# Optimization experiments

Hardware: AMD Instinct MI355X
Metric: run time of the kernel (lower is better)

Reference implementation:

```python
import jax, jax.numpy as jnp
import numpy as np

N = 2048      # agent_num
H = 2048      # hid_size
OBS = 1024    # obs_size
A = 64        # action_dim
ITERS = 3     # comm_iters
B = 1         # batch (structurally 1: original does gate.view(1,n,n))
STD = 0.02


def setup_inputs() -> dict:
    key = jax.random.key(0)
    ks = jax.random.split(key, 10)
    f = lambda k, shp: (jax.random.normal(k, shp, jnp.float32) * STD)
    return {
        "obs": jax.random.normal(ks[0], (B, N, OBS), jnp.float32),
        "alive_mask": jnp.ones((N,), jnp.float32),
        "enc_w": f(ks[1], (H, OBS)),
        "enc_b": jnp.zeros((H,), jnp.float32),
        "g_w": f(ks[2], (N, H)),
        "g_b": jnp.zeros((N,), jnp.float32),
        "w_ih": f(ks[3], (4 * H, H)),
        "w_hh": f(ks[4], (4 * H, H)),
        "b_ih": f(ks[5], (4 * H,)),
        "b_hh": f(ks[6], (4 * H,)),
        "act_w": f(ks[7], (A, H)),
        "act_b": jnp.zeros((A,), jnp.float32),
        "val_w": f(ks[8], (1, H)),
        "val_b": jnp.zeros((1,), jnp.float32),
    }


def reference(obs, alive_mask, enc_w, enc_b, g_w, g_b, w_ih, w_hh,
              b_ih, b_hh, act_w, act_b, val_w, val_b):
    b, n, _ = obs.shape
    hid = enc_w.shape[0]
    # state encoder: tanh(Linear(obs))
    e = jnp.tanh(jnp.einsum('bno,ho->bnh', obs, enc_w) + enc_b)  # (B,n,H)
    h = jnp.zeros((b, n, hid), obs.dtype)
    cell = jnp.zeros((b, n, hid), obs.dtype)
    comm_mask = 1.0 - jnp.eye(n, dtype=obs.dtype)                # (n,n), no self-comm
    n_alive = jnp.sum(alive_mask)
    alive_pair = alive_mask[:, None] * alive_mask[None, :]       # alive[j]*alive[i]
    static_w = comm_mask * alive_pair / (n_alive - 1.0)          # (n,n)

    for it in range(ITERS):
        # hard gate: ceil(sigmoid(g(h)))  -> (B, n_sender, n_receiver)
        gate = jnp.ceil(jax.nn.sigmoid(jnp.einsum('bjh,kh->bjk', h, g_w) + g_b))
        G = gate * static_w                                      # (B,n,n)
        # masked gated broadcast-sum over sender agents j (fused, no (B,n,n,H))
        if it == 0:
            c = jnp.zeros_like(h)
        else:
            c = jnp.einsum('bji,bjh->bih', G, h)
        inp = e + c                                              # (B,n,H)
        # torch.nn.LSTMCell, gate order (i, f, g, o)
        z = (jnp.einsum('bnh,gh->bng', inp, w_ih)
             + jnp.einsum('bnh,gh->bng', h, w_hh) + b_ih + b_hh)
        zi, zf, zg, zo = jnp.split(z, 4, axis=-1)
        cell = jax.nn.sigmoid(zf) * cell + jax.nn.sigmoid(zi) * jnp.tanh(zg)
        h = jax.nn.sigmoid(zo) * jnp.tanh(cell)

    log_p = jax.nn.log_softmax(jnp.einsum('bnh,ah->bna', h, act_w) + act_b, axis=-1)
    value = jnp.einsum('bnh,vh->bnv', h, val_w) + val_b
    return log_p, value
```

## Files before the change

kernel.cpp:

```cpp
#include <hip/hip_runtime.h>
#include <cmath>

#define N_AG 2048
#define HID  2048
#define OBSD 1024
#define ACT  64
#define GATES (4*HID)

typedef short s16x8 __attribute__((ext_vector_type(8)));
typedef short s16x4 __attribute__((ext_vector_type(4)));
typedef float f32x4 __attribute__((ext_vector_type(4)));

__device__ __forceinline__ unsigned short f2bf(float f) {
  union { float f; unsigned u; } v; v.f = f;
  return (unsigned short)((v.u + 0x7FFFu + ((v.u >> 16) & 1u)) >> 16);
}
__device__ __forceinline__ float bf2f(unsigned short u) {
  union { float f; unsigned u; } v; v.u = ((unsigned)u) << 16;
  return v.f;
}
__device__ __forceinline__ float fsigm(float x) {
  return __builtin_amdgcn_rcpf(1.0f + __expf(-x));
}
__device__ __forceinline__ float ftanh(float x) {
  return 2.0f * __builtin_amdgcn_rcpf(1.0f + __expf(-2.0f * x)) - 1.0f;
}

__device__ __forceinline__ void gload16(const unsigned short* g, unsigned short* l) {
  __builtin_amdgcn_global_load_lds(
      (const __attribute__((address_space(1))) void*)g,
      (__attribute__((address_space(3))) void*)l, 16, 0, 0);
}


template <int MODE, int ACCS>
__global__ __launch_bounds__(512, 2) void gemm256(
    const unsigned short* __restrict__ A, const unsigned short* __restrict__ B,
    int K, int lda, int ldb,
    unsigned short* __restrict__ E1b, const float* __restrict__ q,
    const float* __restrict__ bc, float* __restrict__ cell,
    unsigned short* __restrict__ hN,
    const float* __restrict__ alive, float* __restrict__ S)
{
  __shared__ __align__(16) unsigned short As[32768];
  __shared__ __align__(16) unsigned short Bs[32768];

  const int tid  = threadIdx.x;
  const int lane = tid & 63;
  const int wave = tid >> 6;
  const int wm   = wave >> 2, wn = wave & 3;
  const int quad = lane >> 4, l16 = lane & 15, r7 = lane & 7;
  const long tileM = (long)blockIdx.y * 256;
  const long tileN = (long)blockIdx.x * 256;

  const unsigned scol  = (((lane & 7) ^ (lane >> 3)) * 8u);
  const unsigned aoffL = (unsigned)(tileM + wave * 8 + (lane >> 3)) * (unsigned)lda + scol;
  const unsigned boffL = (unsigned)(tileN + (wave >> 2) * 64 + (wave & 3) * 8 + (lane >> 3))
                           * (unsigned)ldb + scol;

#define ST_A(d, h, t) { \
    gload16(A + aoffL + (unsigned)((h) * 64) * (unsigned)lda + (unsigned)(t) * 64u, \
            &As[(d) * 16384 + (h) * 8192 + wave * 512]); \
    gload16(A + aoffL + (unsigned)(128 + (h) * 64) * (unsigned)lda + (unsigned)(t) * 64u, \
            &As[(d) * 16384 + (h) * 8192 + wave * 512 + 4096]); }
#define ST_B(d, h, t) { \
    gload16(B + boffL + (unsigned)((h) * 32) * (unsigned)ldb + (unsigned)(t) * 64u, \
            &Bs[(d) * 16384 + (h) * 8192 + wave * 512]); \
    gload16(B + boffL + (unsigned)(128 + (h) * 32) * (unsigned)ldb + (unsigned)(t) * 64u, \
            &Bs[(d) * 16384 + (h) * 8192 + wave * 512 + 4096]); }

  const int ax = wm * 4096 + l16 * 64;
  const int bx = wn * 2048 + l16 * 64;
  const int c0 = (quad ^ r7) * 8;
  const int c1 = ((4 + quad) ^ r7) * 8;

  s16x8 af0[4][2], af1[4][2], bA[2][2], bB[2][2];
  f32x4 acc[8][4] = {};

#define LD_A(d, Mh, dst) { const unsigned short* p_ = &As[(d) * 16384 + (Mh) * 8192 + ax]; \
    _Pragma("unroll") for (int ml = 0; ml < 4; ++ml) { \
      dst[ml][0] = *(const s16x8*)(p_ + ml * 1024 + c0); \
      dst[ml][1] = *(const s16x8*)(p_ + ml * 1024 + c1); } }
#define LD_B(d, Nh, dst) { const unsigned short* p_ = &Bs[(d) * 16384 + (Nh) * 8192 + bx]; \
    _Pragma("unroll") for (int nl = 0; nl < 2; ++nl) { \
      dst[nl][0] = *(const s16x8*)(p_ + nl * 1024 + c0); \
      dst[nl][1] = *(const s16x8*)(p_ + nl * 1024 + c1); } }
#define QMM(Mh, Nh, afv, bb) \
    _Pragma("unroll") for (int ks = 0; ks < 2; ++ks) \
    _Pragma("unroll") for (int ml = 0; ml < 4; ++ml) \
    _Pragma("unroll") for (int nl = 0; nl < 2; ++nl) \
      acc[(Mh) * 4 + ml][(Nh) * 2 + nl] = __builtin_amdgcn_mfma_f32_16x16x32_bf16( \
          afv[ml][ks], bb[nl][ks], acc[(Mh) * 4 + ml][(Nh) * 2 + nl], 0, 0, 0);
#define BAR  __builtin_amdgcn_s_barrier()
#define SCHB __builtin_amdgcn_sched_barrier(0)

  const int NT = K >> 6;

  ST_B(0, 0, 0); ST_A(0, 0, 0); ST_B(0, 1, 0); ST_A(0, 1, 0);
  asm volatile("s_waitcnt vmcnt(0)" ::: "memory");
  BAR;
  LD_A(0, 0, af0); LD_B(0, 0, bA);

  for (int t = 0; t < NT; ++t) {
    const int cur = t & 1, nxt = cur ^ 1;
    const bool s1 = (t + 1 < NT);
    LD_B(cur, 1, bB);
    if (s1) { ST_B(nxt, 0, t + 1); ST_A(nxt, 0, t + 1); }
    SCHB;
    __builtin_amdgcn_s_setprio(1); QMM(0, 0, af0, bA); __builtin_amdgcn_s_setprio(0);
    if (s1) { asm volatile("s_waitcnt vmcnt(4)" ::: "memory"); }
    else    { asm volatile("s_waitcnt vmcnt(0)" ::: "memory"); }
    BAR;
    LD_A(cur, 1, af1);
    if (s1) ST_B(nxt, 1, t + 1);
    SCHB;
    __builtin_amdgcn_s_setprio(1); QMM(0, 1, af0, bB); __builtin_amdgcn_s_setprio(0);
    if (s1) { asm volatile("s_waitcnt vmcnt(2)" ::: "memory"); }
    BAR;
    if (s1) ST_A(nxt, 1, t + 1);
    SCHB;
    __builtin_amdgcn_s_setprio(1); QMM(1, 0, af1, bA); __builtin_amdgcn_s_setprio(0);
    if (s1) LD_B(nxt, 0, bA);
    BAR;
    if (s1) LD_A(nxt, 0, af0);
    SCHB;
    __builtin_amdgcn_s_setprio(1); QMM(1, 1, af1, bB); __builtin_amdgcn_s_setprio(0);
    if (s1) { asm volatile("s_waitcnt vmcnt(2)" ::: "memory"); }
    BAR;
  }

  const int cb0 = (int)tileN + wn * 64;
  const int hid = ((cb0 >> 6) << 4) | l16;
  const int bid = (int)blockIdx.y * (int)gridDim.x + (int)blockIdx.x;
  float bcv[4], qv[4];
#pragma unroll
  for (int g = 0; g < 4; ++g) {
    bcv[g] = bc[cb0 + g * 16 + l16];
    qv[g]  = (MODE == 11) ? q[cb0 + g * 16 + l16] : 0.f;
  }
  float sacc = 0.f;
#pragma unroll
  for (int mf = 0; mf < 8; ++mf) {
    long ag0 = tileM + wm * 128 + mf * 16 + quad * 4;
#pragma unroll
    for (int r = 0; r < 4; ++r) {
      long ag = ag0 + r;
      const size_t pk = ((size_t)bid * 32 + (mf * 4 + r)) * 512 + tid;
      float zi = acc[mf][0][r], zf = acc[mf][1][r];
      float zg = acc[mf][2][r], zo = acc[mf][3][r];
      if (MODE == 10) {
        s16x4 ev;
        ev[0] = (short)f2bf(zi); ev[1] = (short)f2bf(zf);
        ev[2] = (short)f2bf(zg); ev[3] = (short)f2bf(zo);
        *(s16x4*)&E1b[pk * 4] = ev;
        zi += bcv[0]; zf += bcv[1]; zg += bcv[2]; zo += bcv[3];
      } else {
        s16x4 ev = *(const s16x4*)&E1b[pk * 4];
        zi += bf2f((unsigned short)ev[0]) + qv[0] + bcv[0];
        zf += bf2f((unsigned short)ev[1]) + qv[1] + bcv[1];
        zg += bf2f((unsigned short)ev[2]) + qv[2] + bcv[2];
        zo += bf2f((unsigned short)ev[3]) + qv[3] + bcv[3];
      }
      float cold = (MODE == 10) ? 0.f : cell[pk];
      float cnew = fsigm(zf) * cold + fsigm(zi) * ftanh(zg);
      float hv   = fsigm(zo) * ftanh(cnew);
      cell[pk] = cnew;
      hN[(size_t)ag * HID + hid] = f2bf(hv);
      if (ACCS) sacc += alive[ag] * hv;
    }
  }
  if (ACCS) {
    sacc += __shfl_xor(sacc, 16);
    sacc += __shfl_xor(sacc, 32);
    if (quad == 0) atomicAdd(&S[hid], sacc);
  }
#undef ST_A
#undef ST_B
#undef LD_A
#undef LD_B
#undef QMM
#undef BAR
#undef SCHB
}

template <int MODE>
__global__ __launch_bounds__(256, 4) void gemm_bt(
    const unsigned short* __restrict__ A, const unsigned short* __restrict__ B,
    int K, int lda, int ldb,
    unsigned short* __restrict__ Cb, float* __restrict__ Cf, int ldc,
    const float* __restrict__ bias)
{
  __shared__ __align__(16) unsigned short As0[2 * 128 * 32];
  __shared__ __align__(16) unsigned short Bs0[2 * 128 * 32];
  const int tid  = threadIdx.x;
  const int lane = tid & 63;
  const int wave = tid >> 6;
  const int wm = wave >> 1, wn = wave & 1;
  const int quad = lane >> 4, l16 = lane & 15;
  const long tileM = (long)blockIdx.y * 128;
  const long tileN = (long)blockIdx.x * 128;
  const long koff  = (long)blockIdx.z * K;

  const int srow = lane >> 2;
  const int skc  = (lane & 3) * 8;
  const unsigned short* gA = &A[(tileM + wave * 32 + srow) * lda + koff + skc];
  const unsigned short* gB = &B[(tileN + wave * 32 + srow) * ldb + koff + skc];
  const int ldsOff = wave * 32 * 32;

  f32x4 acc[4][4] = {};
  const int nIt = K >> 5;

  gload16(gA, &As0[ldsOff]);
  gload16(gA + 16 * lda, &As0[ldsOff + 16 * 32]);
  gload16(gB, &Bs0[ldsOff]);
  gload16(gB + 16 * ldb, &Bs0[ldsOff + 16 * 32]);

  for (int i = 0; i < nIt; ++i) {
    __syncthreads();
    const int cb = (i & 1) * 4096;
    if (i + 1 < nIt) {
      const int nb = ((i + 1) & 1) * 4096;
      const long ko = (long)(i + 1) * 32;
      gload16(gA + ko, &As0[nb + ldsOff]);
      gload16(gA + ko + 16 * lda, &As0[nb + ldsOff + 16 * 32]);
      gload16(gB + ko, &Bs0[nb + ldsOff]);
      gload16(gB + ko + 16 * ldb, &Bs0[nb + ldsOff + 16 * 32]);
    }
    s16x8 af[4], bfr[4];
#pragma unroll
    for (int ii = 0; ii < 4; ++ii)
      af[ii] = *(const s16x8*)&As0[cb + (wm * 64 + ii * 16 + l16) * 32 + quad * 8];
#pragma unroll
    for (int j = 0; j < 4; ++j)
      bfr[j] = *(const s16x8*)&Bs0[cb + (wn * 64 + j * 16 + l16) * 32 + quad * 8];
#pragma unroll
    for (int ii = 0; ii < 4; ++ii)
#pragma unroll
      for (int j = 0; j < 4; ++j)
        acc[ii][j] = __builtin_amdgcn_mfma_f32_16x16x32_bf16(af[ii], bfr[j], acc[ii][j], 0, 0, 0);
  }

#pragma unroll
  for (int i = 0; i < 4; ++i) {
    long r0 = tileM + wm * 64 + i * 16 + quad * 4;
#pragma unroll
    for (int j = 0; j < 4; ++j) {
      long col = tileN + wn * 64 + j * 16 + l16;
      float bv = (MODE == 1) ? bias[col] : 0.f;
#pragma unroll
      for (int r = 0; r < 4; ++r) {
        float v = acc[i][j][r];
        if (MODE == 1) { v = ftanh(v + bv); Cb[(r0 + r) * ldc + col] = f2bf(v); }
        if (MODE == 2) atomicAdd(&Cf[(r0 + r) * ldc + col], v);
      }
    }
  }
}

__global__ void cvt4_dual(const float* __restrict__ inA, unsigned short* __restrict__ outA,
                          const float* __restrict__ inB, unsigned short* __restrict__ outB) {
  int i = blockIdx.x * 256 + threadIdx.x;
  f32x4 a = ((const f32x4*)inA)[i];
  f32x4 b = ((const f32x4*)inB)[i];
  s16x4 oa, ob;
#pragma unroll
  for (int c = 0; c < 4; ++c) { oa[c] = (short)f2bf(a[c]); ob[c] = (short)f2bf(b[c]); }
  ((s16x4*)outA)[i] = oa;
  ((s16x4*)outB)[i] = ob;
}

__global__ void buildw(const float* __restrict__ w_ih, const float* __restrict__ w_hh,
                       const float* __restrict__ nA,
                       unsigned short* __restrict__ Wihb, unsigned short* __restrict__ W2b) {
  int i = blockIdx.x * 256 + threadIdx.x;
  float s = 1.0f / (nA[0] - 1.0f);
  int c  = i >> 9;
  int kk = (i & 511) * 4;
  int g   = (c >> 4) & 3;
  int hid = ((c >> 6) << 4) | (c & 15);
  size_t src = ((size_t)g * HID + hid) * HID + kk;
  size_t dst = (size_t)c * HID + kk;
  f32x4 a = *(const f32x4*)&w_ih[src];
  f32x4 b = *(const f32x4*)&w_hh[src];
  s16x4 oa, ob;
#pragma unroll
  for (int e = 0; e < 4; ++e) {
    oa[e] = (short)f2bf(a[e]);
    ob[e] = (short)f2bf(b[e] - s * a[e]);
  }
  *(s16x4*)&Wihb[dst] = oa;
  *(s16x4*)&W2b[dst] = ob;
}

__global__ void build_whd(const float* __restrict__ act_w, const float* __restrict__ val_w,
                          unsigned short* __restrict__ whd) {
  int i = blockIdx.x * 256 + threadIdx.x;
  int r = i >> 9;
  int k = (i & 511) * 4;
  f32x4 v = {0.f, 0.f, 0.f, 0.f};
  if (r < 64)       v = *(const f32x4*)&act_w[(size_t)r * HID + k];
  else if (r == 64) v = *(const f32x4*)&val_w[k];
  s16x4 o;
  o[0] = (short)f2bf(v[0]); o[1] = (short)f2bf(v[1]);
  o[2] = (short)f2bf(v[2]); o[3] = (short)f2bf(v[3]);
  *(s16x4*)&whd[(size_t)r * HID + k] = o;
}

__global__ void biasmix(const float* __restrict__ b_ih, const float* __restrict__ b_hh,
                        float* __restrict__ bc) {
  int i = blockIdx.x * 256 + threadIdx.x;
  if (i < GATES) {
    int g   = (i >> 4) & 3;
    int hid = ((i >> 6) << 4) | (i & 15);
    int src = g * HID + hid;
    bc[i] = b_ih[src] + b_hh[src];
  }
}

__global__ void nalive_k(const float* __restrict__ alive, float* __restrict__ nA) {
  __shared__ float red[256];
  float s = 0.f;
  for (int i = threadIdx.x; i < N_AG; i += 256) s += alive[i];
  red[threadIdx.x] = s;
  __syncthreads();
  for (int st = 128; st > 0; st >>= 1) {
    if (threadIdx.x < st) red[threadIdx.x] += red[threadIdx.x + st];
    __syncthreads();
  }
  if (threadIdx.x == 0) nA[0] = red[0];
}

__global__ __launch_bounds__(256) void gemv_q(const unsigned short* __restrict__ Wihb,
                                              const float* __restrict__ S,
                                              const float* __restrict__ nA,
                                              float* __restrict__ q) {
  __shared__ float Sl[HID];
  int tid = threadIdx.x, lane = tid & 63, wave = tid >> 6;
  for (int k = tid; k < HID; k += 256) Sl[k] = S[k];
  __syncthreads();
  int g = blockIdx.x * 4 + wave;
  const unsigned short* wr = Wihb + (size_t)g * HID;
  float acc = 0.f;
#pragma unroll
  for (int c = 0; c < 4; ++c) {
    int k = c * 512 + lane * 8;
    s16x8 w = *(const s16x8*)&wr[k];
#pragma unroll
    for (int e = 0; e < 8; ++e) acc += bf2f((unsigned short)w[e]) * Sl[k + e];
  }
  for (int off = 32; off; off >>= 1) acc += __shfl_xor(acc, off);
  if (lane == 0) q[g] = acc / (nA[0] - 1.0f);
}

__global__ __launch_bounds__(256) void head_ep(const float* __restrict__ zh,
                                               const float* __restrict__ act_b,
                                               const float* __restrict__ val_b,
                                               float* __restrict__ out) {
  int wave = threadIdx.x >> 6, lane = threadIdx.x & 63;
  int row = blockIdx.x * 4 + wave;
  const float* zr = zh + (size_t)row * 128;
  float a = zr[lane] + act_b[lane];
  float m = a;
  for (int off = 32; off; off >>= 1) m = fmaxf(m, __shfl_xor(m, off));
  float ex = expf(a - m), s = ex;
  for (int off = 32; off; off >>= 1) s += __shfl_xor(s, off);
  out[(size_t)row * ACT + lane] = a - m - logf(s);
  if (lane == 0) out[(size_t)N_AG * ACT + row] = zr[64] + val_b[0];
}

extern "C" void kernel_launch(void* const* d_in, const int* in_sizes, int n_in,
                              void* d_out, int out_size, void* d_ws, size_t ws_size,
                              hipStream_t stream) {
  const float* obs   = (const float*)d_in[0];
  const float* alive = (const float*)d_in[1];
  const float* enc_w = (const float*)d_in[2];
  const float* enc_b = (const float*)d_in[3];
  const float* w_ih  = (const float*)d_in[6];
  const float* w_hh  = (const float*)d_in[7];
  const float* b_ih  = (const float*)d_in[8];
  const float* b_hh  = (const float*)d_in[9];
  const float* act_w = (const float*)d_in[10];
  const float* act_b = (const float*)d_in[11];
  const float* val_w = (const float*)d_in[12];
  const float* val_b = (const float*)d_in[13];
  float* out = (float*)d_out;

  char* p = (char*)d_ws;
  unsigned short* Wihb = (unsigned short*)p; p += (size_t)GATES * HID * 2;
  unsigned short* W2b  = (unsigned short*)p; p += (size_t)GATES * HID * 2;
  unsigned short* E1b  = (unsigned short*)p; p += (size_t)N_AG * GATES * 2;
  unsigned short* obsb = (unsigned short*)p; p += (size_t)N_AG * OBSD * 2;
  unsigned short* encb = (unsigned short*)p; p += (size_t)HID * OBSD * 2;
  unsigned short* eb   = (unsigned short*)p; p += (size_t)N_AG * HID * 2;
  unsigned short* h0   = (unsigned short*)p; p += (size_t)N_AG * HID * 2;
  unsigned short* h1   = (unsigned short*)p; p += (size_t)N_AG * HID * 2;
  unsigned short* Whd  = (unsigned short*)p; p += (size_t)128 * HID * 2;
  float* cell = (float*)p; p += (size_t)N_AG * HID * 4;
  float* zh   = (float*)p; p += (size_t)N_AG * 128 * 4;
  float* bc   = (float*)p; p += GATES * 4;
  float* q    = (float*)p; p += GATES * 4;
  float* S12  = (float*)p; p += 2 * HID * 4;
  float* nA   = (float*)p; p += 256;
  float* S1 = S12, *S2 = S12 + HID;

  cvt4_dual<<<(N_AG * OBSD / 4) / 256, 256, 0, stream>>>(obs, obsb, enc_w, encb);
  nalive_k<<<1, 256, 0, stream>>>(alive, nA);
  buildw<<<((size_t)GATES * HID / 4) / 256, 256, 0, stream>>>(w_ih, w_hh, nA, Wihb, W2b);
  build_whd<<<(128 * HID / 4) / 256, 256, 0, stream>>>(act_w, val_w, Whd);
  biasmix<<<GATES / 256, 256, 0, stream>>>(b_ih, b_hh, bc);
  hipMemsetAsync(S12, 0, 2 * HID * 4, stream);
  hipMemsetAsync(zh, 0, (size_t)N_AG * 128 * 4, stream);

  gemm_bt<1><<<dim3(HID / 128, N_AG / 128), 256, 0, stream>>>(
      obsb, encb, OBSD, OBSD, OBSD, eb, nullptr, HID, enc_b);

  gemm256<10, 1><<<dim3(GATES / 256, N_AG / 256), 512, 0, stream>>>(
      eb, Wihb, HID, HID, HID, E1b, nullptr, bc, cell, h0, alive, S1);

  gemv_q<<<GATES / 4, 256, 0, stream>>>(Wihb, S1, nA, q);
  gemm256<11, 1><<<dim3(GATES / 256, N_AG / 256), 512, 0, stream>>>(
      h0, W2b, HID, HID, HID, E1b, q, bc, cell, h1, alive, S2);

  gemv_q<<<GATES / 4, 256, 0, stream>>>(Wihb, S2, nA, q);
  gemm256<11, 0><<<dim3(GATES / 256, N_AG / 256), 512, 0, stream>>>(
      h1, W2b, HID, HID, HID, E1b, q, bc, cell, h0, alive, nullptr);

  gemm_bt<2><<<dim3(1, N_AG / 128, 8), 256, 0, stream>>>(
      h0, Whd, HID / 8, HID, HID, nullptr, zh, 128, nullptr);
  head_ep<<<N_AG / 4, 256, 0, stream>>>(zh, act_b, val_b, out);
}
```

Measured before the change: 477.6 us.

## Fuse prep kernels, swizzle block order, stage h stores through LDS

Merges the conversion, weight-build, bias-mix and memset launches into one prep kernel to cut launch overhead. Remaps block indices in gemm256 and the encoder GEMM so consecutive blocks share the same B (weight) tile, aiming for better L2 reuse. The LSTM epilogue now writes h into LDS and then emits coalesced 16-byte row stores instead of scattered 2-byte stores. The LDS staging adds a barrier and reuses the A buffer after the main loop.

```diff
diff --git a/kernel.cpp b/kernel.cpp
--- a/kernel.cpp
+++ b/kernel.cpp
@@ -50,8 +50,9 @@
   const int wave = tid >> 6;
   const int wm   = wave >> 2, wn = wave & 3;
   const int quad = lane >> 4, l16 = lane & 15, r7 = lane & 7;
-  const long tileM = (long)blockIdx.y * 256;
-  const long tileN = (long)blockIdx.x * 256;
+  const int lin  = (int)blockIdx.x + (int)blockIdx.y * (int)gridDim.x;
+  const long tileM = (long)(lin & 7) * 256;
+  const long tileN = (long)(lin >> 3) * 256;
 
   const unsigned scol  = (((lane & 7) ^ (lane >> 3)) * 8u);
   const unsigned aoffL = (unsigned)(tileM + wave * 8 + (lane >> 3)) * (unsigned)lda + scol;
@@ -130,14 +131,15 @@
   }
 
   const int cb0 = (int)tileN + wn * 64;
-  const int hid = ((cb0 >> 6) << 4) | l16;
-  const int bid = (int)blockIdx.y * (int)gridDim.x + (int)blockIdx.x;
+  const int hid0 = (int)(tileN >> 2);
+  const int bid = lin;
   float bcv[4], qv[4];
 #pragma unroll
   for (int g = 0; g < 4; ++g) {
     bcv[g] = bc[cb0 + g * 16 + l16];
     qv[g]  = (MODE == 11) ? q[cb0 + g * 16 + l16] : 0.f;
   }
+  unsigned short* hlds = As;
   float sacc = 0.f;
 #pragma unroll
   for (int mf = 0; mf < 8; ++mf) {
@@ -165,14 +167,22 @@
       float cnew = fsigm(zf) * cold + fsigm(zi) * ftanh(zg);
       float hv   = fsigm(zo) * ftanh(cnew);
       cell[pk] = cnew;
-      hN[(size_t)ag * HID + hid] = f2bf(hv);
+      hlds[(wm * 128 + mf * 16 + quad * 4 + r) * 64 + (wn * 16 + l16)] = f2bf(hv);
       if (ACCS) sacc += alive[ag] * hv;
     }
   }
   if (ACCS) {
     sacc += __shfl_xor(sacc, 16);
     sacc += __shfl_xor(sacc, 32);
-    if (quad == 0) atomicAdd(&S[hid], sacc);
+    if (quad == 0) atomicAdd(&S[hid0 + wn * 16 + l16], sacc);
+  }
+  __syncthreads();
+#pragma unroll
+  for (int k2 = 0; k2 < 4; ++k2) {
+    int ci = tid + 512 * k2;
+    int row = ci >> 3, c8 = ci & 7;
+    s16x8 v = *(const s16x8*)&hlds[ci * 8];
+    *(s16x8*)&hN[(tileM + row) * HID + hid0 + c8 * 8] = v;
   }
 #undef ST_A
 #undef ST_B
@@ -197,8 +207,14 @@
   const int wave = tid >> 6;
   const int wm = wave >> 1, wn = wave & 1;
   const int quad = lane >> 4, l16 = lane & 15;
-  const long tileM = (long)blockIdx.y * 128;
-  const long tileN = (long)blockIdx.x * 128;
+  int bxs = (int)blockIdx.x, bys = (int)blockIdx.y;
+  if (MODE == 1) {
+    int lin = (int)blockIdx.x + (int)blockIdx.y * (int)gridDim.x;
+    bys = lin % (int)gridDim.y;
+    bxs = lin / (int)gridDim.y;
+  }
+  const long tileM = (long)bys * 128;
+  const long tileN = (long)bxs * 128;
   const long koff  = (long)blockIdx.z * K;
 
   const int srow = lane >> 2;
@@ -257,63 +273,77 @@
   }
 }
 
-__global__ void cvt4_dual(const float* __restrict__ inA, unsigned short* __restrict__ outA,
-                          const float* __restrict__ inB, unsigned short* __restrict__ outB) {
-  int i = blockIdx.x * 256 + threadIdx.x;
-  f32x4 a = ((const f32x4*)inA)[i];
-  f32x4 b = ((const f32x4*)inB)[i];
-  s16x4 oa, ob;
-#pragma unroll
-  for (int c = 0; c < 4; ++c) { oa[c] = (short)f2bf(a[c]); ob[c] = (short)f2bf(b[c]); }
-  ((s16x4*)outA)[i] = oa;
-  ((s16x4*)outB)[i] = ob;
-}
-
-__global__ void buildw(const float* __restrict__ w_ih, const float* __restrict__ w_hh,
-                       const float* __restrict__ nA,
-                       unsigned short* __restrict__ Wihb, unsigned short* __restrict__ W2b) {
-  int i = blockIdx.x * 256 + threadIdx.x;
-  float s = 1.0f / (nA[0] - 1.0f);
-  int c  = i >> 9;
-  int kk = (i & 511) * 4;
-  int g   = (c >> 4) & 3;
-  int hid = ((c >> 6) << 4) | (c & 15);
-  size_t src = ((size_t)g * HID + hid) * HID + kk;
-  size_t dst = (size_t)c * HID + kk;
-  f32x4 a = *(const f32x4*)&w_ih[src];
-  f32x4 b = *(const f32x4*)&w_hh[src];
-  s16x4 oa, ob;
-#pragma unroll
-  for (int e = 0; e < 4; ++e) {
-    oa[e] = (short)f2bf(a[e]);
-    ob[e] = (short)f2bf(b[e] - s * a[e]);
-  }
-  *(s16x4*)&Wihb[dst] = oa;
-  *(s16x4*)&W2b[dst] = ob;
-}
-
-__global__ void build_whd(const float* __restrict__ act_w, const float* __restrict__ val_w,
-                          unsigned short* __restrict__ whd) {
-  int i = blockIdx.x * 256 + threadIdx.x;
-  int r = i >> 9;
-  int k = (i & 511) * 4;
-  f32x4 v = {0.f, 0.f, 0.f, 0.f};
-  if (r < 64)       v = *(const f32x4*)&act_w[(size_t)r * HID + k];
-  else if (r == 64) v = *(const f32x4*)&val_w[k];
-  s16x4 o;
-  o[0] = (short)f2bf(v[0]); o[1] = (short)f2bf(v[1]);
-  o[2] = (short)f2bf(v[2]); o[3] = (short)f2bf(v[3]);
-  *(s16x4*)&whd[(size_t)r * HID + k] = o;
-}
-
-__global__ void biasmix(const float* __restrict__ b_ih, const float* __restrict__ b_hh,
-                        float* __restrict__ bc) {
-  int i = blockIdx.x * 256 + threadIdx.x;
-  if (i < GATES) {
+#define PB_BUILDW  16384
+#define PB_CVT     2048
+#define PB_WHD     256
+#define PB_BIAS    32
+#define PB_ZH      256
+#define PB_S       4
+#define PB_TOTAL   (PB_BUILDW + PB_CVT + PB_WHD + PB_BIAS + PB_ZH + PB_S)
+__global__ void prep(const float* __restrict__ w_ih, const float* __restrict__ w_hh,
+                     const float* __restrict__ nA,
+                     unsigned short* __restrict__ Wihb, unsigned short* __restrict__ W2b,
+                     const float* __restrict__ obs, unsigned short* __restrict__ obsb,
+                     const float* __restrict__ enc_w, unsigned short* __restrict__ encb,
+                     const float* __restrict__ act_w, const float* __restrict__ val_w,
+                     unsigned short* __restrict__ whd,
+                     const float* __restrict__ b_ih, const float* __restrict__ b_hh,
+                     float* __restrict__ bc, float* __restrict__ zh,
+                     float* __restrict__ S12) {
+  int b = blockIdx.x;
+  if (b < PB_BUILDW) {
+    int i = b * 256 + threadIdx.x;
+    float s = 1.0f / (nA[0] - 1.0f);
+    int c  = i >> 9;
+    int kk = (i & 511) * 4;
+    int g   = (c >> 4) & 3;
+    int hid = ((c >> 6) << 4) | (c & 15);
+    size_t src = ((size_t)g * HID + hid) * HID + kk;
+    size_t dst = (size_t)c * HID + kk;
+    f32x4 a = *(const f32x4*)&w_ih[src];
+    f32x4 bb = *(const f32x4*)&w_hh[src];
+    s16x4 oa, ob;
+#pragma unroll
+    for (int e = 0; e < 4; ++e) {
+      oa[e] = (short)f2bf(a[e]);
+      ob[e] = (short)f2bf(bb[e] - s * a[e]);
+    }
+    *(s16x4*)&Wihb[dst] = oa;
+    *(s16x4*)&W2b[dst] = ob;
+  } else if (b < PB_BUILDW + PB_CVT) {
+    int i = (b - PB_BUILDW) * 256 + threadIdx.x;
+    f32x4 a = ((const f32x4*)obs)[i];
+    f32x4 bb = ((const f32x4*)enc_w)[i];
+    s16x4 oa, ob;
+#pragma unroll
+    for (int c = 0; c < 4; ++c) { oa[c] = (short)f2bf(a[c]); ob[c] = (short)f2bf(bb[c]); }
+    ((s16x4*)obsb)[i] = oa;
+    ((s16x4*)encb)[i] = ob;
+  } else if (b < PB_BUILDW + PB_CVT + PB_WHD) {
+    int i = (b - PB_BUILDW - PB_CVT) * 256 + threadIdx.x;
+    int r = i >> 9;
+    int k = (i & 511) * 4;
+    f32x4 v = {0.f, 0.f, 0.f, 0.f};
+    if (r < 64)       v = *(const f32x4*)&act_w[(size_t)r * HID + k];
+    else if (r == 64) v = *(const f32x4*)&val_w[k];
+    s16x4 o;
+    o[0] = (short)f2bf(v[0]); o[1] = (short)f2bf(v[1]);
+    o[2] = (short)f2bf(v[2]); o[3] = (short)f2bf(v[3]);
+    *(s16x4*)&whd[(size_t)r * HID + k] = o;
+  } else if (b < PB_BUILDW + PB_CVT + PB_WHD + PB_BIAS) {
+    int i = (b - PB_BUILDW - PB_CVT - PB_WHD) * 256 + threadIdx.x;
     int g   = (i >> 4) & 3;
     int hid = ((i >> 6) << 4) | (i & 15);
     int src = g * HID + hid;
     bc[i] = b_ih[src] + b_hh[src];
+  } else if (b < PB_BUILDW + PB_CVT + PB_WHD + PB_BIAS + PB_ZH) {
+    int i = (b - PB_BUILDW - PB_CVT - PB_WHD - PB_BIAS) * 256 + threadIdx.x;
+    f32x4 z = {0.f, 0.f, 0.f, 0.f};
+    ((f32x4*)zh)[i] = z;
+  } else {
+    int i = (b - PB_BUILDW - PB_CVT - PB_WHD - PB_BIAS - PB_ZH) * 256 + threadIdx.x;
+    f32x4 z = {0.f, 0.f, 0.f, 0.f};
+    ((f32x4*)S12)[i] = z;
   }
 }
 
@@ -403,13 +433,9 @@
   float* nA   = (float*)p; p += 256;
   float* S1 = S12, *S2 = S12 + HID;
 
-  cvt4_dual<<<(N_AG * OBSD / 4) / 256, 256, 0, stream>>>(obs, obsb, enc_w, encb);
   nalive_k<<<1, 256, 0, stream>>>(alive, nA);
-  buildw<<<((size_t)GATES * HID / 4) / 256, 256, 0, stream>>>(w_ih, w_hh, nA, Wihb, W2b);
-  build_whd<<<(128 * HID / 4) / 256, 256, 0, stream>>>(act_w, val_w, Whd);
-  biasmix<<<GATES / 256, 256, 0, stream>>>(b_ih, b_hh, bc);
-  hipMemsetAsync(S12, 0, 2 * HID * 4, stream);
-  hipMemsetAsync(zh, 0, (size_t)N_AG * 128 * 4, stream);
+  prep<<<PB_TOTAL, 256, 0, stream>>>(w_ih, w_hh, nA, Wihb, W2b, obs, obsb, enc_w, encb,
+                                     act_w, val_w, Whd, b_ih, b_hh, bc, zh, S12);
 
   gemm_bt<1><<<dim3(HID / 128, N_AG / 128), 256, 0, stream>>>(
       obsb, encb, OBSD, OBSD, OBSD, eb, nullptr, HID, enc_b);
```

New measurement: 500.2 us. 1.05x slower.
